# Optimization experiments

Hardware: AMD Instinct MI355X
Metric: run time of the kernel (lower is better)

Reference implementation:

```python
import jax, jax.numpy as jnp
import numpy as np

N, D, M = 100000, 128, 2048


def setup_inputs() -> dict:
    key = jax.random.key(0)
    k1, k2, k3, k4 = jax.random.split(key, 4)
    X = jax.random.normal(k1, (N, D), dtype=jnp.float32)
    Y = jax.random.normal(k2, (N, 1), dtype=jnp.float32)
    centers = jax.random.normal(k3, (M, D), dtype=jnp.float32)
    # alpha is a buffer produced by an inner Falkon solve; use small random values
    alpha = jax.random.normal(k4, (M, 1), dtype=jnp.float32) * 0.01
    sigma = jnp.asarray(1.0, dtype=jnp.float32)     # Gaussian kernel lengthscale (nn.Parameter)
    penalty = jnp.asarray(5.0, dtype=jnp.float32)   # lambda = exp(-penalty)
    return {"X": X, "Y": Y, "centers": centers, "alpha": alpha,
            "sigma": sigma, "penalty": penalty}


def _rbf_mmv(A, B, v, sigma):
    # Gaussian (RBF) kernel mat-vec: exp(-||a-b||^2 / (2 sigma^2)) @ v
    # A:[n,d], B:[m,d], v:[m,1] -> [n,1]
    a2 = jnp.sum(A * A, axis=-1, keepdims=True)          # [n,1]
    b2 = jnp.sum(B * B, axis=-1, keepdims=True).T        # [1,m]
    sq = a2 + b2 - 2.0 * (A @ B.T)                       # [n,m] squared distances
    Kmat = jnp.exp(-sq / (2.0 * sigma * sigma))
    return Kmat @ v


def reference(X, Y, centers, alpha, sigma, penalty):
    # loss = mean((K_NM @ alpha - Y)^2) + exp(-penalty) * alpha^T K_MM alpha
    preds = _rbf_mmv(X, centers, alpha, sigma)                     # [N,1]
    loss = jnp.mean((preds - Y) ** 2)
    pen = jnp.exp(-penalty)
    reg = pen * (alpha.T @ _rbf_mmv(centers, centers, alpha, sigma))  # [1,1]
    total = loss + reg[0, 0]
    return total, preds
```

## Files before the change

kernel.cpp:

```cpp
#include <hip/hip_runtime.h>
#include <stdint.h>

typedef short short8 __attribute__((ext_vector_type(8)));
typedef float f32x4 __attribute__((ext_vector_type(4)));

#define TILE 128
#define BCOLS 64

__device__ __forceinline__ unsigned short f32_to_bf16(float f) {
    uint32_t u = __builtin_bit_cast(uint32_t, f);
    u += 0x7FFFu + ((u >> 16) & 1u);
    return (unsigned short)(u >> 16);
}
__device__ __forceinline__ float bf16_to_f32(unsigned short h) {
    return __builtin_bit_cast(float, (uint32_t)h << 16);
}

typedef const __attribute__((address_space(1))) uint32_t guint;
typedef __attribute__((address_space(3))) uint32_t luint;
__device__ __forceinline__ void dma16(const void* g, void* l) {
    __builtin_amdgcn_global_load_lds((guint*)g, (luint*)l, 16, 0, 0);
}

__global__ void prep_kernel(const float* __restrict__ C,
                            const float* __restrict__ alpha,
                            const float* __restrict__ sigma,
                            unsigned short* __restrict__ Bp,
                            float2* __restrict__ cw,
                            float* __restrict__ acc)
{
    const int t = threadIdx.x;
    const int g = blockIdx.x;
    const int r = t >> 4;
    const int c16 = t & 15;
    const int R = g * 16 + r;

    if (g == 0 && t == 0) {
        acc[0] = 0.f; acc[1] = 0.f;
        ((unsigned int*)acc)[2] = 0u;
    }

    const float4* src = (const float4*)(C + (size_t)R * 128 + c16 * 8);
    float4 va = src[0], vb = src[1];
    unsigned short h[8];
    h[0] = f32_to_bf16(va.x); h[1] = f32_to_bf16(va.y);
    h[2] = f32_to_bf16(va.z); h[3] = f32_to_bf16(va.w);
    h[4] = f32_to_bf16(vb.x); h[5] = f32_to_bf16(vb.y);
    h[6] = f32_to_bf16(vb.z); h[7] = f32_to_bf16(vb.w);
    float ss = 0.f;
    #pragma unroll
    for (int k = 0; k < 8; ++k) {
        float f = bf16_to_f32(h[k]);
        ss = fmaf(f, f, ss);
    }
    uint4 pk;
    pk.x = (uint32_t)h[0] | ((uint32_t)h[1] << 16);
    pk.y = (uint32_t)h[2] | ((uint32_t)h[3] << 16);
    pk.z = (uint32_t)h[4] | ((uint32_t)h[5] << 16);
    pk.w = (uint32_t)h[6] | ((uint32_t)h[7] << 16);
    *reinterpret_cast<uint4*>(Bp + (size_t)g * 2048 + c16 * 128 + r * 8) = pk;

    ss += __shfl_xor(ss, 1);
    ss += __shfl_xor(ss, 2);
    ss += __shfl_xor(ss, 4);
    ss += __shfl_xor(ss, 8);
    if (c16 == 0) {
        float sig = sigma[0];
        float q = 0.7213475204444817f / (sig * sig);
        cw[R] = make_float2(ss * q, alpha[R]);
    }
}

__global__ __launch_bounds__(512, 4)
void fused_kernel(const float* __restrict__ X, int N,
                  const float* __restrict__ Yv,
                  const unsigned short* __restrict__ Bp,
                  const float2* __restrict__ cw,
                  const float* __restrict__ alpha,
                  const float* __restrict__ sigma,
                  const float* __restrict__ penalty,
                  int nA, int nMt, int nBlk,
                  float* __restrict__ preds_out,
                  float* __restrict__ out0,
                  float* __restrict__ acc)
{
    __shared__ __align__(16) unsigned short ldsB[2][8192];
    __shared__ float a2p[TILE][4];
    __shared__ float predbuf[TILE][2];
    __shared__ __align__(16) float rtl[TILE];

    const int t    = threadIdx.x;
    const int lane = t & 63;
    const int wid  = t >> 6;
    const int wr   = wid >> 1;
    const int wc   = wid & 1;
    const int l15  = lane & 15;
    const int quad = lane >> 4;

    const float sig = sigma[0];
    const float q  = 0.7213475204444817f / (sig * sig);
    const float q2 = 2.0f * q;

    const bool regmode = (int)blockIdx.x >= nA;
    int rowbase;
    short8 a[8];

    if (!regmode) {
        rowbase = blockIdx.x * TILE;
        const int r_  = t >> 2;
        const int qtr = t & 3;
        const int grow = rowbase + r_;
        unsigned short* dstbase = &ldsB[0][0] + (r_ >> 4) * 2048 + (r_ & 15) * 8;
        float ss = 0.f;
        if (grow < N) {
            const float4* src = (const float4*)(X + (size_t)grow * 128 + qtr * 32);
            #pragma unroll
            for (int c = 0; c < 4; ++c) {
                float4 va = src[2 * c], vb = src[2 * c + 1];
                unsigned short h0 = f32_to_bf16(va.x), h1 = f32_to_bf16(va.y);
                unsigned short h2 = f32_to_bf16(va.z), h3 = f32_to_bf16(va.w);
                unsigned short h4 = f32_to_bf16(vb.x), h5 = f32_to_bf16(vb.y);
                unsigned short h6 = f32_to_bf16(vb.z), h7 = f32_to_bf16(vb.w);
                float f0 = bf16_to_f32(h0), f1 = bf16_to_f32(h1);
                float f2 = bf16_to_f32(h2), f3 = bf16_to_f32(h3);
                float f4 = bf16_to_f32(h4), f5 = bf16_to_f32(h5);
                float f6 = bf16_to_f32(h6), f7 = bf16_to_f32(h7);
                ss = fmaf(f0, f0, ss); ss = fmaf(f1, f1, ss);
                ss = fmaf(f2, f2, ss); ss = fmaf(f3, f3, ss);
                ss = fmaf(f4, f4, ss); ss = fmaf(f5, f5, ss);
                ss = fmaf(f6, f6, ss); ss = fmaf(f7, f7, ss);
                uint4 pk;
                pk.x = (uint32_t)h0 | ((uint32_t)h1 << 16);
                pk.y = (uint32_t)h2 | ((uint32_t)h3 << 16);
                pk.z = (uint32_t)h4 | ((uint32_t)h5 << 16);
                pk.w = (uint32_t)h6 | ((uint32_t)h7 << 16);
                *reinterpret_cast<uint4*>(dstbase + (qtr * 4 + c) * 128) = pk;
            }
        } else {
            uint4 z; z.x = z.y = z.z = z.w = 0u;
            #pragma unroll
            for (int c = 0; c < 4; ++c)
                *reinterpret_cast<uint4*>(dstbase + (qtr * 4 + c) * 128) = z;
        }
        a2p[r_][qtr] = ss;
        __syncthreads();
        if (t < TILE)
            rtl[t] = -0.5f * (a2p[t][0] + a2p[t][1] + a2p[t][2] + a2p[t][3]);
        const unsigned short* aLds = &ldsB[0][0] + (size_t)(wr * 2) * 2048 + lane * 8;
        #pragma unroll
        for (int i = 0; i < 2; ++i)
            #pragma unroll
            for (int kk = 0; kk < 4; ++kk)
                a[i * 4 + kk] = *reinterpret_cast<const short8*>(aLds + (size_t)i * 2048 + kk * 512);
        __syncthreads();
    } else {
        const int b2 = (int)blockIdx.x - nA;
        rowbase = b2 * TILE;
        const unsigned short* aG = Bp + (size_t)(b2 * 8 + wr * 2) * 2048 + lane * 8;
        #pragma unroll
        for (int i = 0; i < 2; ++i)
            #pragma unroll
            for (int kk = 0; kk < 4; ++kk)
                a[i * 4 + kk] = *reinterpret_cast<const short8*>(aG + (size_t)i * 2048 + kk * 512);
        const float inv_q2 = 0.5f / q;
        if (t < TILE)
            rtl[t] = -cw[rowbase + t].x * inv_q2;
    }

    float srow[2][4] = {};
    const float2* cwb = cw + wc * 32 + l15;
    const float* rtlp = &rtl[wr * 32 + quad * 4];

    const int ldq = wid * 1024 + lane * 8;

    {
        const unsigned short* g = Bp + ldq;
        unsigned short* l = &ldsB[0][0] + ldq;
        #pragma unroll
        for (int k = 0; k < 2; ++k)
            dma16(g + k * 512, l + k * 512);
    }
    __syncthreads();

    for (int mt = 0; mt < nMt; ++mt) {
        if (mt + 1 < nMt) {
            const unsigned short* g = Bp + (size_t)(mt + 1) * 8192 + ldq;
            unsigned short* l = &ldsB[(mt + 1) & 1][0] + ldq;
            #pragma unroll
            for (int k = 0; k < 2; ++k)
                dma16(g + k * 512, l + k * 512);
        }

        float2 cj[2];
        #pragma unroll
        for (int j = 0; j < 2; ++j) cj[j] = cwb[(size_t)mt * 64 + j * 16];

        const unsigned short* bfr = &ldsB[mt & 1][0] + (size_t)(wc * 2) * 2048 + lane * 8;
        #pragma unroll
        for (int j = 0; j < 2; ++j) {
            short8 b[4];
            #pragma unroll
            for (int kk = 0; kk < 4; ++kk)
                b[kk] = *reinterpret_cast<const short8*>(bfr + (size_t)j * 2048 + kk * 512);

            f32x4 acc4[2];
            acc4[0] = *reinterpret_cast<const f32x4*>(rtlp);
            acc4[1] = *reinterpret_cast<const f32x4*>(rtlp + 16);
            #pragma unroll
            for (int kk = 0; kk < 4; ++kk)
                #pragma unroll
                for (int i = 0; i < 2; ++i)
                    acc4[i] = __builtin_amdgcn_mfma_f32_16x16x32_bf16(
                        a[i * 4 + kk], b[kk], acc4[i], 0, 0, 0);

            #pragma unroll
            for (int i = 0; i < 2; ++i) {
                #pragma unroll
                for (int r = 0; r < 4; ++r) {
                    float u = fmaf(acc4[i][r], q2, -cj[j].x);
                    float e = __builtin_amdgcn_exp2f(u);
                    srow[i][r] = fmaf(e, cj[j].y, srow[i][r]);
                }
            }
        }

        __syncthreads();
    }

    #pragma unroll
    for (int i = 0; i < 2; ++i) {
        #pragma unroll
        for (int r = 0; r < 4; ++r) {
            int rl = wr * 32 + i * 16 + quad * 4 + r;
            float v = srow[i][r];
            v += __shfl_xor(v, 1);
            v += __shfl_xor(v, 2);
            v += __shfl_xor(v, 4);
            v += __shfl_xor(v, 8);
            if (l15 == 0)
                predbuf[rl][wc] = v;
        }
    }
    __syncthreads();

    float contrib = 0.f;
    if (t < TILE) {
        int grow = rowbase + t;
        if (!regmode) {
            if (grow < N) {
                float pred = predbuf[t][0] + predbuf[t][1];
                preds_out[grow] = pred;
                float d = pred - Yv[grow];
                contrib = d * d;
            }
        } else {
            float pred = predbuf[t][0] + predbuf[t][1];
            contrib = alpha[grow] * pred;
        }
    }
    contrib += __shfl_xor(contrib, 1);
    contrib += __shfl_xor(contrib, 2);
    contrib += __shfl_xor(contrib, 4);
    contrib += __shfl_xor(contrib, 8);
    contrib += __shfl_xor(contrib, 16);
    contrib += __shfl_xor(contrib, 32);
    if (lane == 0 && wid < 2) atomicAdd(regmode ? (acc + 1) : (acc + 0), contrib);

    __syncthreads();
    if (t == 0) {
        __threadfence();
        unsigned int old = atomicAdd((unsigned int*)(acc + 2), 1u);
        if (old == (unsigned int)(nBlk - 1)) {
            float lv = atomicAdd(acc + 0, 0.0f);
            float rv = atomicAdd(acc + 1, 0.0f);
            out0[0] = lv / (float)N + __expf(-penalty[0]) * rv;
        }
    }
}

extern "C" void kernel_launch(void* const* d_in, const int* in_sizes, int n_in,
                              void* d_out, int out_size, void* d_ws, size_t ws_size,
                              hipStream_t stream) {
    const float* X       = (const float*)d_in[0];
    const float* Y       = (const float*)d_in[1];
    const float* centers = (const float*)d_in[2];
    const float* alpha   = (const float*)d_in[3];
    const float* sigma   = (const float*)d_in[4];
    const float* penalty = (const float*)d_in[5];
    float* out = (float*)d_out;

    const int N = in_sizes[1];
    const int M = in_sizes[3];

    unsigned short* Bp = (unsigned short*)d_ws;
    float2* cw = (float2*)((char*)d_ws + (size_t)M * 256);
    float* acc = (float*)((char*)d_ws + (size_t)M * 264);

    prep_kernel<<<M / 16, 256, 0, stream>>>(centers, alpha, sigma, Bp, cw, acc);

    const int nA  = (N + TILE - 1) / TILE;
    const int nMt = M / BCOLS;
    const int nBlk = nA + M / TILE;
    fused_kernel<<<nBlk, 512, 0, stream>>>(X, N, Y, Bp, cw, alpha, sigma, penalty,
                                           nA, nMt, nBlk, out + 1, out, acc);
}
```

Baseline: 176.4 us.

## Remap waves to 16 rows x 64 cols each, fold row norm into registers

Changes the wave tiling from a 4x2 grid (32 rows x 32 cols per wave) to 8 waves of 16 rows each covering all 64 columns of the center tile. The row norm term now lives in per-lane registers and is folded into the exp argument, so the accumulator no longer has to be seeded from LDS. The cross-wave column reduction through shared memory also goes away. In exchange, each wave loads the full B tile from LDS (twice the LDS read traffic per MFMA) and does one MFMA chain per column group instead of two interleaved ones, which may expose more MFMA latency.

```diff
diff --git a/kernel.cpp b/kernel.cpp
--- a/kernel.cpp
+++ b/kernel.cpp
@@ -86,14 +86,11 @@
 {
     __shared__ __align__(16) unsigned short ldsB[2][8192];
     __shared__ float a2p[TILE][4];
-    __shared__ float predbuf[TILE][2];
-    __shared__ __align__(16) float rtl[TILE];
+    __shared__ float predbuf[TILE];
 
     const int t    = threadIdx.x;
     const int lane = t & 63;
     const int wid  = t >> 6;
-    const int wr   = wid >> 1;
-    const int wc   = wid & 1;
     const int l15  = lane & 15;
     const int quad = lane >> 4;
 
@@ -103,7 +100,8 @@
 
     const bool regmode = (int)blockIdx.x >= nA;
     int rowbase;
-    short8 a[8];
+    float rowterm[4];
+    short8 a[4];
 
     if (!regmode) {
         rowbase = blockIdx.x * TILE;
@@ -144,32 +142,30 @@
         }
         a2p[r_][qtr] = ss;
         __syncthreads();
-        if (t < TILE)
-            rtl[t] = -0.5f * (a2p[t][0] + a2p[t][1] + a2p[t][2] + a2p[t][3]);
-        const unsigned short* aLds = &ldsB[0][0] + (size_t)(wr * 2) * 2048 + lane * 8;
-        #pragma unroll
-        for (int i = 0; i < 2; ++i)
-            #pragma unroll
-            for (int kk = 0; kk < 4; ++kk)
-                a[i * 4 + kk] = *reinterpret_cast<const short8*>(aLds + (size_t)i * 2048 + kk * 512);
+        #pragma unroll
+        for (int r = 0; r < 4; ++r) {
+            int rl = wid * 16 + quad * 4 + r;
+            rowterm[r] = (a2p[rl][0] + a2p[rl][1] + a2p[rl][2] + a2p[rl][3]) * q;
+        }
+        const unsigned short* aLds = &ldsB[0][0] + (size_t)wid * 2048 + lane * 8;
+        #pragma unroll
+        for (int kk = 0; kk < 4; ++kk)
+            a[kk] = *reinterpret_cast<const short8*>(aLds + kk * 512);
         __syncthreads();
     } else {
         const int b2 = (int)blockIdx.x - nA;
         rowbase = b2 * TILE;
-        const unsigned short* aG = Bp + (size_t)(b2 * 8 + wr * 2) * 2048 + lane * 8;
-        #pragma unroll
-        for (int i = 0; i < 2; ++i)
-            #pragma unroll
-            for (int kk = 0; kk < 4; ++kk)
-                a[i * 4 + kk] = *reinterpret_cast<const short8*>(aG + (size_t)i * 2048 + kk * 512);
-        const float inv_q2 = 0.5f / q;
-        if (t < TILE)
-            rtl[t] = -cw[rowbase + t].x * inv_q2;
-    }
-
-    float srow[2][4] = {};
-    const float2* cwb = cw + wc * 32 + l15;
-    const float* rtlp = &rtl[wr * 32 + quad * 4];
+        const unsigned short* aG = Bp + (size_t)(b2 * 8 + wid) * 2048 + lane * 8;
+        #pragma unroll
+        for (int kk = 0; kk < 4; ++kk)
+            a[kk] = *reinterpret_cast<const short8*>(aG + kk * 512);
+        #pragma unroll
+        for (int r = 0; r < 4; ++r)
+            rowterm[r] = cw[rowbase + wid * 16 + quad * 4 + r].x;
+    }
+
+    float srow[4][4] = {};
+    const float2* cwb = cw + l15;
 
     const int ldq = wid * 1024 + lane * 8;
 
@@ -191,36 +187,25 @@
                 dma16(g + k * 512, l + k * 512);
         }
 
-        float2 cj[2];
-        #pragma unroll
-        for (int j = 0; j < 2; ++j) cj[j] = cwb[(size_t)mt * 64 + j * 16];
-
-        const unsigned short* bfr = &ldsB[mt & 1][0] + (size_t)(wc * 2) * 2048 + lane * 8;
-        #pragma unroll
-        for (int j = 0; j < 2; ++j) {
+        const unsigned short* bfr = &ldsB[mt & 1][0] + lane * 8;
+        #pragma unroll
+        for (int j = 0; j < 4; ++j) {
+            float2 cj = cwb[(size_t)mt * 64 + j * 16];
             short8 b[4];
             #pragma unroll
             for (int kk = 0; kk < 4; ++kk)
                 b[kk] = *reinterpret_cast<const short8*>(bfr + (size_t)j * 2048 + kk * 512);
 
-            f32x4 acc4[2];
-            acc4[0] = *reinterpret_cast<const f32x4*>(rtlp);
-            acc4[1] = *reinterpret_cast<const f32x4*>(rtlp + 16);
+            f32x4 acc4 = (f32x4){0.f, 0.f, 0.f, 0.f};
             #pragma unroll
             for (int kk = 0; kk < 4; ++kk)
-                #pragma unroll
-                for (int i = 0; i < 2; ++i)
-                    acc4[i] = __builtin_amdgcn_mfma_f32_16x16x32_bf16(
-                        a[i * 4 + kk], b[kk], acc4[i], 0, 0, 0);
-
-            #pragma unroll
-            for (int i = 0; i < 2; ++i) {
-                #pragma unroll
-                for (int r = 0; r < 4; ++r) {
-                    float u = fmaf(acc4[i][r], q2, -cj[j].x);
-                    float e = __builtin_amdgcn_exp2f(u);
-                    srow[i][r] = fmaf(e, cj[j].y, srow[i][r]);
-                }
+                acc4 = __builtin_amdgcn_mfma_f32_16x16x32_bf16(a[kk], b[kk], acc4, 0, 0, 0);
+
+            #pragma unroll
+            for (int r = 0; r < 4; ++r) {
+                float u = fmaf(acc4[r], q2, -(rowterm[r] + cj.x));
+                float e = __builtin_amdgcn_exp2f(u);
+                srow[j][r] = fmaf(e, cj.y, srow[j][r]);
             }
         }
 
@@ -228,18 +213,14 @@
     }
 
     #pragma unroll
-    for (int i = 0; i < 2; ++i) {
-        #pragma unroll
-        for (int r = 0; r < 4; ++r) {
-            int rl = wr * 32 + i * 16 + quad * 4 + r;
-            float v = srow[i][r];
-            v += __shfl_xor(v, 1);
-            v += __shfl_xor(v, 2);
-            v += __shfl_xor(v, 4);
-            v += __shfl_xor(v, 8);
-            if (l15 == 0)
-                predbuf[rl][wc] = v;
-        }
+    for (int r = 0; r < 4; ++r) {
+        float v = (srow[0][r] + srow[1][r]) + (srow[2][r] + srow[3][r]);
+        v += __shfl_xor(v, 1);
+        v += __shfl_xor(v, 2);
+        v += __shfl_xor(v, 4);
+        v += __shfl_xor(v, 8);
+        if (l15 == 0)
+            predbuf[wid * 16 + quad * 4 + r] = v;
     }
     __syncthreads();
 
@@ -248,14 +229,13 @@
         int grow = rowbase + t;
         if (!regmode) {
             if (grow < N) {
-                float pred = predbuf[t][0] + predbuf[t][1];
+                float pred = predbuf[t];
                 preds_out[grow] = pred;
                 float d = pred - Yv[grow];
                 contrib = d * d;
             }
         } else {
-            float pred = predbuf[t][0] + predbuf[t][1];
-            contrib = alpha[grow] * pred;
+            contrib = alpha[grow] * predbuf[t];
         }
     }
     contrib += __shfl_xor(contrib, 1);
```

Result: slower. 191.3 us (+8.4%).
